# Performance work log

Hardware: AMD Instinct MI355X
Metric: run time of the kernel (lower is better)

Reference implementation:

```python
import jax, jax.numpy as jnp
import numpy as np

B = 65536
SHARED_DIMS = [(937, 512), (512, 512), (512, 256), (256, 256), (256, 256), (256, 256), (256, 256)]
HEAD_DIMS_V = [(256, 128), (128, 64), (64, 1)]
HEAD_DIMS_A = [(256, 128), (128, 64), (64, 4)]


def _init_params(key, dims, prefix):
    out = {}
    for i, (fi, fo) in enumerate(dims):
        key, k1, k2 = jax.random.split(key, 3)
        s = 1.0 / np.sqrt(fi)
        out[f"{prefix}w{i+1}"] = jax.random.uniform(k1, (fi, fo), jnp.float32, -s, s)
        out[f"{prefix}b{i+1}"] = jax.random.uniform(k2, (fo,), jnp.float32, -s, s)
    return out, key


def setup_inputs() -> dict:
    key = jax.random.key(0)
    k1, k2, k3, key = jax.random.split(key, 4)
    inp = {
        "x": jax.random.normal(k1, (B, 937), jnp.float32),
        "suicides": jax.random.randint(k2, (B, 4), 0, 2).astype(bool),
        "invalid_actions": jax.random.randint(k3, (B,), 0, 4),
    }
    p, key = _init_params(key, SHARED_DIMS, "s")
    inp.update(p)
    p, key = _init_params(key, HEAD_DIMS_V, "v")
    inp.update(p)
    p, key = _init_params(key, HEAD_DIMS_A, "a")
    inp.update(p)
    return inp


def _mlp_relu_all(h, ws_bs):
    # Linear+ReLU after every layer (shared trunk ends with ReLU)
    for w, b in ws_bs:
        h = jax.nn.relu(h @ w + b)
    return h


def _head(h, ws_bs):
    # ReLU after all but last layer
    for w, b in ws_bs[:-1]:
        h = jax.nn.relu(h @ w + b)
    w, b = ws_bs[-1]
    return h @ w + b


def reference(x, suicides, invalid_actions,
              sw1, sb1, sw2, sb2, sw3, sb3, sw4, sb4, sw5, sb5, sw6, sb6, sw7, sb7,
              vw1, vb1, vw2, vb2, vw3, vb3,
              aw1, ab1, aw2, ab2, aw3, ab3):
    h = _mlp_relu_all(x, [(sw1, sb1), (sw2, sb2), (sw3, sb3), (sw4, sb4), (sw5, sb5), (sw6, sb6), (sw7, sb7)])
    values = _head(h, [(vw1, vb1), (vw2, vb2), (vw3, vb3)])          # [B,1]
    adv = _head(h, [(aw1, ab1), (aw2, ab2), (aw3, ab3)])             # [B,4]

    all_s = jnp.all(suicides, axis=1)                                 # [B]
    onehot_inv = jnp.arange(4)[None, :] == invalid_actions[:, None]   # [B,4]
    # if all suicides: only the invalid action is masked, denom=3
    # else: suicide actions masked, denom = #non-suicide actions
    mask = jnp.where(all_s[:, None], onehot_inv, suicides)            # [B,4]
    denom = jnp.where(all_s, 3.0, jnp.sum(~suicides, axis=1).astype(jnp.float32))
    means = jnp.sum(jnp.where(mask, 0.0, adv), axis=1) / denom        # [B]
    adv_masked = jnp.where(mask, -jnp.inf, adv)
    return values + (adv_masked - means[:, None])                     # [B,4]
```

## Files before the change

### kernel.cpp

```cpp
#include <hip/hip_runtime.h>
#include <hip/hip_bf16.h>

typedef __attribute__((ext_vector_type(8))) short short8;
typedef __attribute__((ext_vector_type(4))) float f32x4;

#define B_ROWS 65536

__device__ inline unsigned short f2bf(float v) {
    __hip_bfloat16 h = __float2bfloat16(v);
    unsigned short u;
    __builtin_memcpy(&u, &h, 2);
    return u;
}

__device__ inline float bf2f(unsigned short u) {
    union { unsigned int i; float f; } cv;
    cv.i = ((unsigned int)u) << 16;
    return cv.f;
}

__global__ void convert_x_kernel(const float* __restrict__ x, __hip_bfloat16* __restrict__ xb) {
    const int total = B_ROWS * 120;
    for (int i = blockIdx.x * blockDim.x + threadIdx.x; i < total; i += gridDim.x * blockDim.x) {
        int row = i / 120;
        int g = i - row * 120;
        int c0 = g * 8;
        const float* xr = x + (size_t)row * 937;
        short8 r;
#pragma unroll
        for (int j = 0; j < 8; ++j) {
            int c = c0 + j;
            float v = (c < 937) ? xr[c] : 0.0f;
            r[j] = (short)f2bf(v);
        }
        *(short8*)((char*)xb + (size_t)row * 1920 + (size_t)c0 * 2) = r;
    }
}

struct WDesc { const float* src; __hip_bfloat16* dst; int N, K, Npad, Kpad; };
struct WDescs { WDesc d[10]; };

__global__ void prep_weights_kernel(WDescs descs) {
    WDesc w = descs.d[blockIdx.y];
    int kg_count = w.Kpad >> 3;
    int per = w.Npad * kg_count;
    for (int i = blockIdx.x * blockDim.x + threadIdx.x; i < per; i += gridDim.x * blockDim.x) {
        int n = i % w.Npad;
        int kg = i / w.Npad;
        int k0 = kg << 3;
        short8 r;
#pragma unroll
        for (int j = 0; j < 8; ++j) {
            int k = k0 + j;
            float v = (n < w.N && k < w.K) ? w.src[(size_t)k * w.N + n] : 0.0f;
            r[j] = (short)f2bf(v);
        }
        *(short8*)((char*)w.dst + ((size_t)n * w.Kpad + (size_t)k0) * 2) = r;
    }
}

#define BM 128
#define BN 128
#define BK 64

__global__ __launch_bounds__(256) void gemm_bias_relu(
    const __hip_bfloat16* __restrict__ A,
    const __hip_bfloat16* __restrict__ Bt,
    const float* __restrict__ bias,
    __hip_bfloat16* __restrict__ C,
    int K, int N, int relu)
{
    __shared__ __attribute__((aligned(16))) __hip_bfloat16 sA[BM][BK];
    __shared__ __attribute__((aligned(16))) __hip_bfloat16 sB[BN][BK];

    const int t = threadIdx.x;
    const int wid = t >> 6;
    const int lane = t & 63;
    const int brow = blockIdx.x * BM;
    const int bcol = blockIdx.y * BN;
    const int wr = wid >> 1, wc = wid & 1;

    f32x4 acc[4][4] = {};

    const __hip_bfloat16* ga = A + (size_t)(brow + (t >> 3)) * K + (t & 7) * 8;
    const __hip_bfloat16* gb = Bt + (size_t)(bcol + (t >> 3)) * K + (t & 7) * 8;

    for (int k0 = 0; k0 < K; k0 += BK) {
#pragma unroll
        for (int it = 0; it < 4; ++it) {
            __builtin_amdgcn_global_load_lds(
                (const __attribute__((address_space(1))) void*)(ga + (size_t)it * 32 * K + k0),
                (__attribute__((address_space(3))) void*)((char*)&sA[0][0] + it * 4096 + wid * 1024),
                16, 0, 0);
            __builtin_amdgcn_global_load_lds(
                (const __attribute__((address_space(1))) void*)(gb + (size_t)it * 32 * K + k0),
                (__attribute__((address_space(3))) void*)((char*)&sB[0][0] + it * 4096 + wid * 1024),
                16, 0, 0);
        }
        __syncthreads();
#pragma unroll
        for (int kk = 0; kk < 2; ++kk) {
            short8 af[4], bfr[4];
#pragma unroll
            for (int m = 0; m < 4; ++m)
                af[m] = *(const short8*)&sA[wr * 64 + m * 16 + (lane & 15)][kk * 32 + (lane >> 4) * 8];
#pragma unroll
            for (int n = 0; n < 4; ++n)
                bfr[n] = *(const short8*)&sB[wc * 64 + n * 16 + (lane & 15)][kk * 32 + (lane >> 4) * 8];
#pragma unroll
            for (int m = 0; m < 4; ++m)
#pragma unroll
                for (int n = 0; n < 4; ++n)
                    acc[m][n] = __builtin_amdgcn_mfma_f32_16x16x32_bf16(af[m], bfr[n], acc[m][n], 0, 0, 0);
        }
        __syncthreads();
    }

    float biasv[4];
#pragma unroll
    for (int n = 0; n < 4; ++n) {
        int col = bcol + wc * 64 + n * 16 + (lane & 15);
        biasv[n] = (col < N) ? bias[col] : 0.0f;
    }
#pragma unroll
    for (int m = 0; m < 4; ++m) {
        int row = brow + wr * 64 + m * 16 + ((lane >> 4) << 2);
#pragma unroll
        for (int n = 0; n < 4; ++n) {
            int col = bcol + wc * 64 + n * 16 + (lane & 15);
            if (col < N) {
#pragma unroll
                for (int r = 0; r < 4; ++r) {
                    float v = acc[m][n][r] + biasv[n];
                    if (relu) v = fmaxf(v, 0.0f);
                    C[(size_t)(row + r) * N + col] = __float2bfloat16(v);
                }
            }
        }
    }
}

__global__ __launch_bounds__(256) void head_final(
    const __hip_bfloat16* __restrict__ hv, const __hip_bfloat16* __restrict__ ha,
    const float* __restrict__ vw3, const float* __restrict__ vb3,
    const float* __restrict__ aw3, const float* __restrict__ ab3,
    const int* __restrict__ suicides, const int* __restrict__ invalid,
    float* __restrict__ out)
{
    __shared__ float svw[64];
    __shared__ float saw[256];
    int t = threadIdx.x;
    if (t < 64) svw[t] = vw3[t];
    saw[t] = aw3[t];
    __syncthreads();

    int lane = t & 63;
    int w = t >> 6;
    int quad = lane & 3;
    int row = blockIdx.x * 64 + w * 16 + (lane >> 2);

    const short8* pv = (const short8*)(hv + (size_t)row * 64 + quad * 16);
    short8 v0 = pv[0], v1 = pv[1];
    const short8* pa = (const short8*)(ha + (size_t)row * 64 + quad * 16);
    short8 a0 = pa[0], a1 = pa[1];

    float vsum = 0.0f;
    float as[4] = {0.0f, 0.0f, 0.0f, 0.0f};
#pragma unroll
    for (int j = 0; j < 8; ++j) {
        int k = quad * 16 + j;
        float hv_f = bf2f((unsigned short)v0[j]);
        float ha_f = bf2f((unsigned short)a0[j]);
        vsum += hv_f * svw[k];
#pragma unroll
        for (int jj = 0; jj < 4; ++jj) as[jj] += ha_f * saw[k * 4 + jj];
    }
#pragma unroll
    for (int j = 0; j < 8; ++j) {
        int k = quad * 16 + 8 + j;
        float hv_f = bf2f((unsigned short)v1[j]);
        float ha_f = bf2f((unsigned short)a1[j]);
        vsum += hv_f * svw[k];
#pragma unroll
        for (int jj = 0; jj < 4; ++jj) as[jj] += ha_f * saw[k * 4 + jj];
    }
    vsum += __shfl_xor(vsum, 1); vsum += __shfl_xor(vsum, 2);
#pragma unroll
    for (int jj = 0; jj < 4; ++jj) {
        as[jj] += __shfl_xor(as[jj], 1);
        as[jj] += __shfl_xor(as[jj], 2);
    }

    if (quad == 0) {
        float value = vsum + vb3[0];
        float adv[4];
#pragma unroll
        for (int jj = 0; jj < 4; ++jj) adv[jj] = as[jj] + ab3[jj];

        int4 sv = *(const int4*)(suicides + (size_t)row * 4);
        int s0 = sv.x != 0, s1 = sv.y != 0, s2 = sv.z != 0, s3 = sv.w != 0;
        int all_s = s0 & s1 & s2 & s3;
        int inv = invalid[row];

        int sarr[4] = {s0, s1, s2, s3};
        bool mask[4];
#pragma unroll
        for (int jj = 0; jj < 4; ++jj)
            mask[jj] = all_s ? (jj == inv) : (sarr[jj] != 0);

        float denom = all_s ? 3.0f : (float)(4 - (s0 + s1 + s2 + s3));
        float sum = 0.0f;
#pragma unroll
        for (int jj = 0; jj < 4; ++jj) if (!mask[jj]) sum += adv[jj];
        float mean = sum / denom;

        float ninf = -1.0e30f;
        float4 o;
        o.x = mask[0] ? ninf : value + adv[0] - mean;
        o.y = mask[1] ? ninf : value + adv[1] - mean;
        o.z = mask[2] ? ninf : value + adv[2] - mean;
        o.w = mask[3] ? ninf : value + adv[3] - mean;
        *(float4*)(out + (size_t)row * 4) = o;
    }
}

extern "C" void kernel_launch(void* const* d_in, const int* in_sizes, int n_in,
                              void* d_out, int out_size, void* d_ws, size_t ws_size,
                              hipStream_t stream) {
    const float* x = (const float*)d_in[0];
    const int* suicides = (const int*)d_in[1];
    const int* invalid = (const int*)d_in[2];

    char* ws = (char*)d_ws;
    size_t off = 0;
    auto alloc = [&](size_t bytes) { char* p = ws + off; off += (bytes + 255) & ~(size_t)255; return p; };

    __hip_bfloat16* wT1 = (__hip_bfloat16*)alloc((size_t)512 * 960 * 2);
    __hip_bfloat16* wT2 = (__hip_bfloat16*)alloc((size_t)512 * 512 * 2);
    __hip_bfloat16* wT3 = (__hip_bfloat16*)alloc((size_t)256 * 512 * 2);
    __hip_bfloat16* wT4 = (__hip_bfloat16*)alloc((size_t)256 * 256 * 2);
    __hip_bfloat16* wT5 = (__hip_bfloat16*)alloc((size_t)256 * 256 * 2);
    __hip_bfloat16* wT6 = (__hip_bfloat16*)alloc((size_t)256 * 256 * 2);
    __hip_bfloat16* wT7 = (__hip_bfloat16*)alloc((size_t)256 * 256 * 2);
    __hip_bfloat16* wTv1 = (__hip_bfloat16*)alloc((size_t)128 * 256 * 2);
    __hip_bfloat16* wTv2 = (__hip_bfloat16*)alloc((size_t)128 * 128 * 2);
    __hip_bfloat16* wTa1 = (__hip_bfloat16*)alloc((size_t)128 * 256 * 2);
    __hip_bfloat16* wTa2 = (__hip_bfloat16*)alloc((size_t)128 * 128 * 2);

    __hip_bfloat16* actA = (__hip_bfloat16*)alloc((size_t)B_ROWS * 960 * 2);
    __hip_bfloat16* actB = (__hip_bfloat16*)alloc((size_t)B_ROWS * 512 * 2);

    __hip_bfloat16* v1 = actA;
    __hip_bfloat16* v2 = actA + (size_t)B_ROWS * 128;
    __hip_bfloat16* a1 = actA + (size_t)B_ROWS * 192;
    __hip_bfloat16* a2 = actA + (size_t)B_ROWS * 320;

    WDescs descs;
    descs.d[0] = { (const float*)d_in[3],  wT1, 512, 937, 512, 960 };
    descs.d[1] = { (const float*)d_in[5],  wT2, 512, 512, 512, 512 };
    descs.d[2] = { (const float*)d_in[7],  wT3, 256, 512, 256, 512 };
    descs.d[3] = { (const float*)d_in[9],  wT4, 256, 256, 256, 256 };
    descs.d[4] = { (const float*)d_in[11], wT5, 256, 256, 256, 256 };
    descs.d[5] = { (const float*)d_in[13], wT6, 256, 256, 256, 256 };
    descs.d[6] = { (const float*)d_in[15], wT7, 256, 256, 256, 256 };
    descs.d[7] = { (const float*)d_in[17], wTv1, 128, 256, 128, 256 };
    descs.d[8] = { (const float*)d_in[19], wTv2,  64, 128, 128, 128 };
    descs.d[9] = { (const float*)d_in[23], wTa1, 128, 256, 128, 256 };
    prep_weights_kernel<<<dim3(240, 10), 256, 0, stream>>>(descs);
    WDescs descs2;
    descs2.d[0] = { (const float*)d_in[25], wTa2, 64, 128, 128, 128 };
    for (int i = 1; i < 10; ++i) descs2.d[i] = descs2.d[0];
    prep_weights_kernel<<<dim3(8, 1), 256, 0, stream>>>(descs2);

    convert_x_kernel<<<2048, 256, 0, stream>>>(x, actA);

    auto gemm = [&](const __hip_bfloat16* A, const __hip_bfloat16* Bt, const float* bias,
                    __hip_bfloat16* C, int K, int N, int Npad, int relu) {
        dim3 grid(B_ROWS / BM, Npad / BN);
        gemm_bias_relu<<<grid, 256, 0, stream>>>(A, Bt, bias, C, K, N, relu);
    };

    gemm(actA, wT1, (const float*)d_in[4],  actB, 960, 512, 512, 1);
    gemm(actB, wT2, (const float*)d_in[6],  actA, 512, 512, 512, 1);
    gemm(actA, wT3, (const float*)d_in[8],  actB, 512, 256, 256, 1);
    gemm(actB, wT4, (const float*)d_in[10], actA, 256, 256, 256, 1);
    gemm(actA, wT5, (const float*)d_in[12], actB, 256, 256, 256, 1);
    gemm(actB, wT6, (const float*)d_in[14], actA, 256, 256, 256, 1);
    gemm(actA, wT7, (const float*)d_in[16], actB, 256, 256, 256, 1);

    gemm(actB, wTv1, (const float*)d_in[18], v1, 256, 128, 128, 1);
    gemm(v1,   wTv2, (const float*)d_in[20], v2, 128,  64, 128, 1);
    gemm(actB, wTa1, (const float*)d_in[24], a1, 256, 128, 128, 1);
    gemm(a1,   wTa2, (const float*)d_in[26], a2, 128,  64, 128, 1);

    head_final<<<B_ROWS / 64, 256, 0, stream>>>(
        v2, a2,
        (const float*)d_in[21], (const float*)d_in[22],
        (const float*)d_in[27], (const float*)d_in[28],
        suicides, invalid, (float*)d_out);

    (void)in_sizes; (void)n_in; (void)out_size; (void)ws_size;
}
```

Baseline: 895.1 us.

## Fuse trunk layers 4-7 and both heads into one LDS-resident tail kernel

Replaces the last four 256x256 trunk GEMMs, the four head GEMMs and the final head kernel with one fused kernel. Each block keeps a 128-row activation tile in swizzled LDS across six MFMA layers and reads weights straight from global memory. The value and advantage heads are packed into a combined 256-wide layer and a block-diagonal second layer. This removes about nine kernel launches and the global round-trips of intermediate activations, at the cost of 64KB LDS per block, a large accumulator array per thread, and some zero-padding compute. The x conversion is also rewritten to one block per row, staging through LDS.

```diff
diff --git a/kernel.cpp b/kernel.cpp
--- a/kernel.cpp
+++ b/kernel.cpp
@@ -19,26 +19,25 @@
     return cv.f;
 }
 
-__global__ void convert_x_kernel(const float* __restrict__ x, __hip_bfloat16* __restrict__ xb) {
-    const int total = B_ROWS * 120;
-    for (int i = blockIdx.x * blockDim.x + threadIdx.x; i < total; i += gridDim.x * blockDim.x) {
-        int row = i / 120;
-        int g = i - row * 120;
-        int c0 = g * 8;
-        const float* xr = x + (size_t)row * 937;
-        short8 r;
-#pragma unroll
-        for (int j = 0; j < 8; ++j) {
-            int c = c0 + j;
-            float v = (c < 937) ? xr[c] : 0.0f;
-            r[j] = (short)f2bf(v);
-        }
-        *(short8*)((char*)xb + (size_t)row * 1920 + (size_t)c0 * 2) = r;
-    }
+__global__ __launch_bounds__(256) void convert_x_kernel(const float* __restrict__ x,
+                                                        __hip_bfloat16* __restrict__ xb) {
+    __shared__ __attribute__((aligned(16))) unsigned short ls[960];
+    const int r = blockIdx.x;
+    const int t = threadIdx.x;
+    const float* xr = x + (size_t)r * 937;
+#pragma unroll
+    for (int p = 0; p < 4; ++p) {
+        int c = t + p * 256;
+        if (c < 937) ls[c] = f2bf(xr[c]);
+        else if (c < 960) ls[c] = 0;
+    }
+    __syncthreads();
+    if (t < 120)
+        *(short8*)(xb + (size_t)r * 960 + t * 8) = *(const short8*)&ls[t * 8];
 }
 
 struct WDesc { const float* src; __hip_bfloat16* dst; int N, K, Npad, Kpad; };
-struct WDescs { WDesc d[10]; };
+struct WDescs { WDesc d[7]; };
 
 __global__ void prep_weights_kernel(WDescs descs) {
     WDesc w = descs.d[blockIdx.y];
@@ -59,6 +58,41 @@
     }
 }
 
+struct TailArgs {
+    const float *vw1, *vb1, *aw1, *ab1, *vw2, *vb2, *aw2, *ab2;
+    const float *b4, *b5, *b6, *b7;
+    __hip_bfloat16* Wtail;
+    float* Bs;
+};
+
+__global__ void prep_tail_kernel(TailArgs a) {
+    int g = blockIdx.x * 256 + threadIdx.x;
+    int half = g >> 16;
+    int j = g & 65535;
+    int n = j >> 8, k = j & 255;
+    float v;
+    if (half == 0) {
+        v = (n < 128) ? a.vw1[(size_t)k * 128 + n] : a.aw1[(size_t)k * 128 + (n - 128)];
+    } else {
+        if (n < 64 && k < 128)                 v = a.vw2[(size_t)k * 64 + n];
+        else if (n >= 64 && n < 128 && k >= 128) v = a.aw2[(size_t)(k - 128) * 64 + (n - 64)];
+        else                                   v = 0.0f;
+    }
+    a.Wtail[(size_t)(4 + half) * 65536 + j] = __float2bfloat16(v);
+
+    if (g < 1536) {
+        int l = g >> 8, nn = g & 255;
+        float bv;
+        if (l == 0) bv = a.b4[nn];
+        else if (l == 1) bv = a.b5[nn];
+        else if (l == 2) bv = a.b6[nn];
+        else if (l == 3) bv = a.b7[nn];
+        else if (l == 4) bv = (nn < 128) ? a.vb1[nn] : a.ab1[nn - 128];
+        else             bv = (nn < 64) ? a.vb2[nn] : (nn < 128 ? a.ab2[nn - 64] : 0.0f);
+        a.Bs[g] = bv;
+    }
+}
+
 #define BM 128
 #define BN 128
 #define BK 64
@@ -140,69 +174,111 @@
     }
 }
 
-__global__ __launch_bounds__(256) void head_final(
-    const __hip_bfloat16* __restrict__ hv, const __hip_bfloat16* __restrict__ ha,
+
+__device__ __forceinline__ char* swzp(char* base, int row, int byte_in_row) {
+    return base + row * 512 + (byte_in_row ^ ((row & 7) << 4));
+}
+
+__global__ __launch_bounds__(256, 2) void fused_tail(
+    const __hip_bfloat16* __restrict__ h3,
+    const __hip_bfloat16* __restrict__ Wtail,
+    const float* __restrict__ Bs,
     const float* __restrict__ vw3, const float* __restrict__ vb3,
     const float* __restrict__ aw3, const float* __restrict__ ab3,
     const int* __restrict__ suicides, const int* __restrict__ invalid,
     float* __restrict__ out)
 {
+    __shared__ __attribute__((aligned(16))) unsigned char sAct[128 * 512];
     __shared__ float svw[64];
     __shared__ float saw[256];
-    int t = threadIdx.x;
+
+    const int t = threadIdx.x;
+    const int wid = t >> 6;
+    const int lane = t & 63;
+    const int brow = blockIdx.x * 128;
+    const int wnbase = wid * 64;
+
     if (t < 64) svw[t] = vw3[t];
     saw[t] = aw3[t];
+
+    {
+        const __hip_bfloat16* src = h3 + (size_t)brow * 256;
+        int r = t >> 1, c0 = (t & 1) * 128;
+#pragma unroll
+        for (int j = 0; j < 16; ++j) {
+            short8 v = *(const short8*)(src + (size_t)r * 256 + c0 + j * 8);
+            *(short8*)swzp((char*)sAct, r, (c0 + j * 8) * 2) = v;
+        }
+    }
     __syncthreads();
 
-    int lane = t & 63;
-    int w = t >> 6;
-    int quad = lane & 3;
-    int row = blockIdx.x * 64 + w * 16 + (lane >> 2);
-
-    const short8* pv = (const short8*)(hv + (size_t)row * 64 + quad * 16);
-    short8 v0 = pv[0], v1 = pv[1];
-    const short8* pa = (const short8*)(ha + (size_t)row * 64 + quad * 16);
-    short8 a0 = pa[0], a1 = pa[1];
-
-    float vsum = 0.0f;
-    float as[4] = {0.0f, 0.0f, 0.0f, 0.0f};
-#pragma unroll
-    for (int j = 0; j < 8; ++j) {
-        int k = quad * 16 + j;
-        float hv_f = bf2f((unsigned short)v0[j]);
-        float ha_f = bf2f((unsigned short)a0[j]);
-        vsum += hv_f * svw[k];
-#pragma unroll
-        for (int jj = 0; jj < 4; ++jj) as[jj] += ha_f * saw[k * 4 + jj];
-    }
-#pragma unroll
-    for (int j = 0; j < 8; ++j) {
-        int k = quad * 16 + 8 + j;
-        float hv_f = bf2f((unsigned short)v1[j]);
-        float ha_f = bf2f((unsigned short)a1[j]);
-        vsum += hv_f * svw[k];
-#pragma unroll
-        for (int jj = 0; jj < 4; ++jj) as[jj] += ha_f * saw[k * 4 + jj];
-    }
-    vsum += __shfl_xor(vsum, 1); vsum += __shfl_xor(vsum, 2);
-#pragma unroll
-    for (int jj = 0; jj < 4; ++jj) {
-        as[jj] += __shfl_xor(as[jj], 1);
-        as[jj] += __shfl_xor(as[jj], 2);
-    }
-
-    if (quad == 0) {
-        float value = vsum + vb3[0];
-        float adv[4];
-#pragma unroll
-        for (int jj = 0; jj < 4; ++jj) adv[jj] = as[jj] + ab3[jj];
-
-        int4 sv = *(const int4*)(suicides + (size_t)row * 4);
+    for (int layer = 0; layer < 6; ++layer) {
+        const __hip_bfloat16* W = Wtail + (size_t)layer * 65536;
+        const float* bias = Bs + layer * 256;
+
+        f32x4 acc[8][4] = {};
+#pragma unroll
+        for (int kk = 0; kk < 8; ++kk) {
+            short8 bfrag[4];
+#pragma unroll
+            for (int n = 0; n < 4; ++n)
+                bfrag[n] = *(const short8*)(W + (size_t)(wnbase + n * 16 + (lane & 15)) * 256
+                                            + kk * 32 + (lane >> 4) * 8);
+            short8 afrag[8];
+#pragma unroll
+            for (int m = 0; m < 8; ++m) {
+                int r = m * 16 + (lane & 15);
+                afrag[m] = *(const short8*)swzp((char*)sAct, r, (kk * 32 + (lane >> 4) * 8) * 2);
+            }
+#pragma unroll
+            for (int m = 0; m < 8; ++m)
+#pragma unroll
+                for (int n = 0; n < 4; ++n)
+                    acc[m][n] = __builtin_amdgcn_mfma_f32_16x16x32_bf16(afrag[m], bfrag[n], acc[m][n], 0, 0, 0);
+        }
+        __syncthreads();
+
+        float bv[4];
+#pragma unroll
+        for (int n = 0; n < 4; ++n) bv[n] = bias[wnbase + n * 16 + (lane & 15)];
+#pragma unroll
+        for (int m = 0; m < 8; ++m) {
+#pragma unroll
+            for (int n = 0; n < 4; ++n) {
+                int col = wnbase + n * 16 + (lane & 15);
+#pragma unroll
+                for (int r4 = 0; r4 < 4; ++r4) {
+                    int row = m * 16 + ((lane >> 4) << 2) + r4;
+                    float v = fmaxf(acc[m][n][r4] + bv[n], 0.0f);
+                    *(unsigned short*)swzp((char*)sAct, row, col * 2) = f2bf(v);
+                }
+            }
+        }
+        __syncthreads();
+    }
+
+    if (t < 128) {
+        int grow = brow + t;
+        float vsum = vb3[0];
+        float a0 = ab3[0], a1 = ab3[1], a2v = ab3[2], a3v = ab3[3];
+#pragma unroll
+        for (int k = 0; k < 64; ++k) {
+            float hv = bf2f(*(unsigned short*)swzp((char*)sAct, t, k * 2));
+            float ha = bf2f(*(unsigned short*)swzp((char*)sAct, t, (64 + k) * 2));
+            vsum += hv * svw[k];
+            a0 += ha * saw[k * 4 + 0];
+            a1 += ha * saw[k * 4 + 1];
+            a2v += ha * saw[k * 4 + 2];
+            a3v += ha * saw[k * 4 + 3];
+        }
+        float adv[4] = { a0, a1, a2v, a3v };
+
+        int4 sv = *(const int4*)(suicides + (size_t)grow * 4);
         int s0 = sv.x != 0, s1 = sv.y != 0, s2 = sv.z != 0, s3 = sv.w != 0;
         int all_s = s0 & s1 & s2 & s3;
-        int inv = invalid[row];
-
-        int sarr[4] = {s0, s1, s2, s3};
+        int inv = invalid[grow];
+
+        int sarr[4] = { s0, s1, s2, s3 };
         bool mask[4];
 #pragma unroll
         for (int jj = 0; jj < 4; ++jj)
@@ -216,11 +292,11 @@
 
         float ninf = -1.0e30f;
         float4 o;
-        o.x = mask[0] ? ninf : value + adv[0] - mean;
-        o.y = mask[1] ? ninf : value + adv[1] - mean;
-        o.z = mask[2] ? ninf : value + adv[2] - mean;
-        o.w = mask[3] ? ninf : value + adv[3] - mean;
-        *(float4*)(out + (size_t)row * 4) = o;
+        o.x = mask[0] ? ninf : vsum + adv[0] - mean;
+        o.y = mask[1] ? ninf : vsum + adv[1] - mean;
+        o.z = mask[2] ? ninf : vsum + adv[2] - mean;
+        o.w = mask[3] ? ninf : vsum + adv[3] - mean;
+        *(float4*)(out + (size_t)grow * 4) = o;
     }
 }
 
@@ -238,41 +314,33 @@
     __hip_bfloat16* wT1 = (__hip_bfloat16*)alloc((size_t)512 * 960 * 2);
     __hip_bfloat16* wT2 = (__hip_bfloat16*)alloc((size_t)512 * 512 * 2);
     __hip_bfloat16* wT3 = (__hip_bfloat16*)alloc((size_t)256 * 512 * 2);
-    __hip_bfloat16* wT4 = (__hip_bfloat16*)alloc((size_t)256 * 256 * 2);
-    __hip_bfloat16* wT5 = (__hip_bfloat16*)alloc((size_t)256 * 256 * 2);
-    __hip_bfloat16* wT6 = (__hip_bfloat16*)alloc((size_t)256 * 256 * 2);
-    __hip_bfloat16* wT7 = (__hip_bfloat16*)alloc((size_t)256 * 256 * 2);
-    __hip_bfloat16* wTv1 = (__hip_bfloat16*)alloc((size_t)128 * 256 * 2);
-    __hip_bfloat16* wTv2 = (__hip_bfloat16*)alloc((size_t)128 * 128 * 2);
-    __hip_bfloat16* wTa1 = (__hip_bfloat16*)alloc((size_t)128 * 256 * 2);
-    __hip_bfloat16* wTa2 = (__hip_bfloat16*)alloc((size_t)128 * 128 * 2);
+    __hip_bfloat16* Wtail = (__hip_bfloat16*)alloc((size_t)6 * 65536 * 2);
+    float* Bs = (float*)alloc((size_t)6 * 256 * 4);
 
     __hip_bfloat16* actA = (__hip_bfloat16*)alloc((size_t)B_ROWS * 960 * 2);
     __hip_bfloat16* actB = (__hip_bfloat16*)alloc((size_t)B_ROWS * 512 * 2);
 
-    __hip_bfloat16* v1 = actA;
-    __hip_bfloat16* v2 = actA + (size_t)B_ROWS * 128;
-    __hip_bfloat16* a1 = actA + (size_t)B_ROWS * 192;
-    __hip_bfloat16* a2 = actA + (size_t)B_ROWS * 320;
-
     WDescs descs;
-    descs.d[0] = { (const float*)d_in[3],  wT1, 512, 937, 512, 960 };
-    descs.d[1] = { (const float*)d_in[5],  wT2, 512, 512, 512, 512 };
-    descs.d[2] = { (const float*)d_in[7],  wT3, 256, 512, 256, 512 };
-    descs.d[3] = { (const float*)d_in[9],  wT4, 256, 256, 256, 256 };
-    descs.d[4] = { (const float*)d_in[11], wT5, 256, 256, 256, 256 };
-    descs.d[5] = { (const float*)d_in[13], wT6, 256, 256, 256, 256 };
-    descs.d[6] = { (const float*)d_in[15], wT7, 256, 256, 256, 256 };
-    descs.d[7] = { (const float*)d_in[17], wTv1, 128, 256, 128, 256 };
-    descs.d[8] = { (const float*)d_in[19], wTv2,  64, 128, 128, 128 };
-    descs.d[9] = { (const float*)d_in[23], wTa1, 128, 256, 128, 256 };
-    prep_weights_kernel<<<dim3(240, 10), 256, 0, stream>>>(descs);
-    WDescs descs2;
-    descs2.d[0] = { (const float*)d_in[25], wTa2, 64, 128, 128, 128 };
-    for (int i = 1; i < 10; ++i) descs2.d[i] = descs2.d[0];
-    prep_weights_kernel<<<dim3(8, 1), 256, 0, stream>>>(descs2);
-
-    convert_x_kernel<<<2048, 256, 0, stream>>>(x, actA);
+    descs.d[0] = { (const float*)d_in[3],  wT1,              512, 937, 512, 960 };
+    descs.d[1] = { (const float*)d_in[5],  wT2,              512, 512, 512, 512 };
+    descs.d[2] = { (const float*)d_in[7],  wT3,              256, 512, 256, 512 };
+    descs.d[3] = { (const float*)d_in[9],  Wtail + 0 * 65536, 256, 256, 256, 256 };
+    descs.d[4] = { (const float*)d_in[11], Wtail + 1 * 65536, 256, 256, 256, 256 };
+    descs.d[5] = { (const float*)d_in[13], Wtail + 2 * 65536, 256, 256, 256, 256 };
+    descs.d[6] = { (const float*)d_in[15], Wtail + 3 * 65536, 256, 256, 256, 256 };
+    prep_weights_kernel<<<dim3(240, 7), 256, 0, stream>>>(descs);
+
+    TailArgs ta;
+    ta.vw1 = (const float*)d_in[17]; ta.vb1 = (const float*)d_in[18];
+    ta.vw2 = (const float*)d_in[19]; ta.vb2 = (const float*)d_in[20];
+    ta.aw1 = (const float*)d_in[23]; ta.ab1 = (const float*)d_in[24];
+    ta.aw2 = (const float*)d_in[25]; ta.ab2 = (const float*)d_in[26];
+    ta.b4 = (const float*)d_in[10]; ta.b5 = (const float*)d_in[12];
+    ta.b6 = (const float*)d_in[14]; ta.b7 = (const float*)d_in[16];
+    ta.Wtail = Wtail; ta.Bs = Bs;
+    prep_tail_kernel<<<512, 256, 0, stream>>>(ta);
+
+    convert_x_kernel<<<B_ROWS, 256, 0, stream>>>(x, actA);
 
     auto gemm = [&](const __hip_bfloat16* A, const __hip_bfloat16* Bt, const float* bias,
                     __hip_bfloat16* C, int K, int N, int Npad, int relu) {
@@ -280,21 +348,12 @@
         gemm_bias_relu<<<grid, 256, 0, stream>>>(A, Bt, bias, C, K, N, relu);
     };
 
-    gemm(actA, wT1, (const float*)d_in[4],  actB, 960, 512, 512, 1);
-    gemm(actB, wT2, (const float*)d_in[6],  actA, 512, 512, 512, 1);
-    gemm(actA, wT3, (const float*)d_in[8],  actB, 512, 256, 256, 1);
-    gemm(actB, wT4, (const float*)d_in[10], actA, 256, 256, 256, 1);
-    gemm(actA, wT5, (const float*)d_in[12], actB, 256, 256, 256, 1);
-    gemm(actB, wT6, (const float*)d_in[14], actA, 256, 256, 256, 1);
-    gemm(actA, wT7, (const float*)d_in[16], actB, 256, 256, 256, 1);
-
-    gemm(actB, wTv1, (const float*)d_in[18], v1, 256, 128, 128, 1);
-    gemm(v1,   wTv2, (const float*)d_in[20], v2, 128,  64, 128, 1);
-    gemm(actB, wTa1, (const float*)d_in[24], a1, 256, 128, 128, 1);
-    gemm(a1,   wTa2, (const float*)d_in[26], a2, 128,  64, 128, 1);
-
-    head_final<<<B_ROWS / 64, 256, 0, stream>>>(
-        v2, a2,
+    gemm(actA, wT1, (const float*)d_in[4], actB, 960, 512, 512, 1);
+    gemm(actB, wT2, (const float*)d_in[6], actA, 512, 512, 512, 1);
+    gemm(actA, wT3, (const float*)d_in[8], actB, 512, 256, 256, 1);
+
+    fused_tail<<<B_ROWS / 128, 256, 0, stream>>>(
+        actB, Wtail, Bs,
         (const float*)d_in[21], (const float*)d_in[22],
         (const float*)d_in[27], (const float*)d_in[28],
         suicides, invalid, (float*)d_out);
```

New measurement: 825.1 us. -7.8%, faster.
